# Optimization experiments

Hardware: AMD Instinct MI355X
Metric: run time of the kernel (lower is better)

The kernel has to match this reference:

```python
import jax, jax.numpy as jnp
import numpy as np

BATCH, SEQ, IN, HID = 32, 1024, 512, 1024


def setup_inputs() -> dict:
    key = jax.random.key(0)
    std = 1.0 / np.sqrt(HID)
    ks = jax.random.split(key, 16)
    u = lambda k, shape: jax.random.uniform(k, shape, jnp.float32, -std, std)
    return {
        "x": jax.random.normal(ks[0], (BATCH, SEQ, IN), jnp.float32),
        "Wi": u(ks[1], (IN, 2 * HID)),
        "Wh": u(ks[2], (HID, 2 * HID)),
        "B": u(ks[3], (2 * HID,)),
        "Wni": u(ks[4], (IN, HID)),
        "Wnh": u(ks[5], (HID, HID)),
        "Bni": u(ks[6], (HID,)),
        "Bnh": u(ks[7], (HID,)),
        "Winvi": u(ks[8], (IN, 2 * HID)),
        "Winvh": u(ks[9], (HID, 2 * HID)),
        "Binv": u(ks[10], (2 * HID,)),
        "Wninvi": u(ks[11], (IN, HID)),
        "Wninvh": u(ks[12], (HID, HID)),
        "Bninvi": u(ks[13], (HID,)),
        "Bninvh": u(ks[14], (HID,)),
    }


def _gru_scan(x, Wi, Wh, Bg, Wni, Wnh, Bni, Bnh, reverse):
    # x: [B,S,I]; precompute input projections once (same math, batched GEMM)
    H = Wnh.shape[0]
    gi = jnp.einsum('bsi,ig->bsg', x, Wi) + Bg   # [B,S,2H]
    ni = jnp.einsum('bsi,ih->bsh', x, Wni) + Bni # [B,S,H]
    h0 = jnp.zeros((x.shape[0], H), x.dtype)

    def step(h, inp):
        g_t, n_t = inp                        # [B,2H], [B,H]
        gates = g_t + h @ Wh
        r = jax.nn.sigmoid(gates[:, :H])
        z = jax.nn.sigmoid(gates[:, H:])
        n = jnp.tanh(n_t + r * (h @ Wnh + Bnh))
        h = (1 - z) * n + z * h
        return h, h

    hT, hs = jax.lax.scan(step, h0, (gi.swapaxes(0, 1), ni.swapaxes(0, 1)),
                          reverse=reverse)
    return hs.swapaxes(0, 1), hT              # [B,S,H], [B,H]


def reference(x, Wi, Wh, B, Wni, Wnh, Bni, Bnh,
              Winvi, Winvh, Binv, Wninvi, Wninvh, Bninvi, Bninvh):
    out_f, h_f = _gru_scan(x, Wi, Wh, B, Wni, Wnh, Bni, Bnh, reverse=False)
    out_b, h_b = _gru_scan(x, Winvi, Winvh, Binv, Wninvi, Wninvh, Bninvi, Bninvh,
                           reverse=True)
    output = jnp.concatenate([out_f, out_b], axis=-1)  # [B,S,2H]
    ht = jnp.concatenate([h_f, h_b], axis=-1)          # [B,2H]
    return output, ht
```

## Files before the change

kernel.cpp:

```cpp
#include <hip/hip_runtime.h>
#include <cstdint>
#include <cstddef>

typedef __attribute__((ext_vector_type(8))) short s8v;
typedef __attribute__((ext_vector_type(4))) float f4v;
typedef __attribute__((ext_vector_type(4))) unsigned int u4v;

#define DEVFN __device__ __forceinline__

DEVFN unsigned short f2bf(float f) {
    unsigned int u = __builtin_bit_cast(unsigned int, f);
    return (unsigned short)((u + 0x7FFFu + ((u >> 16) & 1u)) >> 16);
}
DEVFN float bf2f(unsigned short h) {
    unsigned int u = ((unsigned int)h) << 16;
    return __builtin_bit_cast(float, u);
}
DEVFN float sigm(float x) { return 1.0f / (1.0f + __expf(-x)); }
DEVFN float tanh_fast(float x) { float e = __expf(2.0f * x); return 1.0f - 2.0f / (e + 1.0f); }

DEVFN u4v pack8(const unsigned short o[8]) {
    u4v v;
    v[0] = (unsigned)o[0] | ((unsigned)o[1] << 16);
    v[1] = (unsigned)o[2] | ((unsigned)o[3] << 16);
    v[2] = (unsigned)o[4] | ((unsigned)o[5] << 16);
    v[3] = (unsigned)o[6] | ((unsigned)o[7] << 16);
    return v;
}

DEVFN void store_wt(unsigned int* p, unsigned int v) {
    asm volatile("global_store_dword %0, %1, off sc0 sc1"
                 :: "v"(p), "v"(v) : "memory");
}
DEVFN unsigned poll_load(const unsigned int* p) {
    unsigned v;
    asm volatile("global_load_dword %0, %1, off sc0 sc1\n\t"
                 "s_waitcnt vmcnt(0)"
                 : "=v"(v) : "v"(p) : "memory");
    return v;
}
DEVFN void gather_h(const void* p0, const void* p1,
                    u4v& a0, u4v& a1, u4v& a2, u4v& a3,
                    u4v& a4, u4v& a5, u4v& a6, u4v& a7) {
    asm volatile(
        "global_load_dwordx4 %0, %8, off sc0 sc1\n\t"
        "global_load_dwordx4 %1, %8, off offset:1024 sc0 sc1\n\t"
        "global_load_dwordx4 %2, %8, off offset:2048 sc0 sc1\n\t"
        "global_load_dwordx4 %3, %8, off offset:3072 sc0 sc1\n\t"
        "global_load_dwordx4 %4, %9, off sc0 sc1\n\t"
        "global_load_dwordx4 %5, %9, off offset:1024 sc0 sc1\n\t"
        "global_load_dwordx4 %6, %9, off offset:2048 sc0 sc1\n\t"
        "global_load_dwordx4 %7, %9, off offset:3072 sc0 sc1\n\t"
        "s_waitcnt vmcnt(0)"
        : "=&v"(a0), "=&v"(a1), "=&v"(a2), "=&v"(a3),
          "=&v"(a4), "=&v"(a5), "=&v"(a6), "=&v"(a7)
        : "v"(p0), "v"(p1)
        : "memory");
}

constexpr int BB = 32, SS = 1024, II = 512, HH = 1024;
constexpr int NCOL = 6144;

constexpr size_t OFF_X    = 0;
constexpr size_t SZ_X     = (size_t)BB * SS * II * 2;
constexpr size_t OFF_WINT = OFF_X + SZ_X;
constexpr size_t SZ_WINT  = (size_t)NCOL * II * 2;
constexpr size_t OFF_WREC = OFF_WINT + SZ_WINT;
constexpr size_t SZ_WREC  = (size_t)2 * 3072 * HH * 2;
constexpr size_t OFF_BIAS = OFF_WREC + SZ_WREC;
constexpr size_t SZ_BIAS  = (size_t)NCOL * 4;
constexpr size_t OFF_H    = OFF_BIAS + SZ_BIAS;
constexpr size_t SZ_H     = (size_t)2 * 2 * 2 * 64 * 512;
constexpr size_t OFF_BAR  = OFF_H + SZ_H;
constexpr size_t SZ_BAR   = 4096;
constexpr size_t OFF_G    = OFF_BAR + SZ_BAR;
constexpr size_t SZ_G     = (size_t)SS * BB * NCOL * 2;
constexpr size_t WS_NEED  = OFF_G + SZ_G;

constexpr int WL_OFF = 0;
constexpr int PL_OFF = 98304;
constexpr int GR_OFF = 124416;
constexpr int PF_OFF = 130560;
constexpr int RD_OFF = 130592;
constexpr int PG_OFF = 130608;
constexpr int SMEM_TOT = 130624;
constexpr int PLF = 4 * 3 * 16 * 17;

__global__ void prep_kernel(
    const float* __restrict__ x,
    const float* __restrict__ Wi, const float* __restrict__ Wni,
    const float* __restrict__ Winvi, const float* __restrict__ Wninvi,
    const float* __restrict__ Wh, const float* __restrict__ Wnh,
    const float* __restrict__ Winvh, const float* __restrict__ Wninvh,
    const float* __restrict__ Bg, const float* __restrict__ Bni,
    const float* __restrict__ Binv, const float* __restrict__ Bninvi,
    unsigned short* __restrict__ xb, unsigned short* __restrict__ WinT,
    unsigned short* __restrict__ Wrec, float* __restrict__ bias)
{
    constexpr int NX8  = (BB * SS * II) / 8;
    constexpr int NWI8 = (NCOL * II) / 8;
    constexpr int NWR8 = (2 * 3072 * HH) / 8;
    constexpr int TOT  = NX8 + NWI8 + NWR8 + NCOL;
    for (int i = blockIdx.x * blockDim.x + threadIdx.x; i < TOT;
         i += gridDim.x * blockDim.x) {
        if (i < NX8) {
            const float* sp = x + (size_t)i * 8;
            unsigned short o[8];
#pragma unroll
            for (int j = 0; j < 8; ++j) o[j] = f2bf(sp[j]);
            *(u4v*)(xb + (size_t)i * 8) = pack8(o);
        } else if (i < NX8 + NWI8) {
            int u = i - NX8;
            int n = u >> 6, k0 = (u & 63) * 8;
            const float* src; int stride;
            if (n < 2048)      { src = Wi + n;            stride = 2048; }
            else if (n < 3072) { src = Wni + (n - 2048);  stride = 1024; }
            else if (n < 5120) { src = Winvi + (n - 3072); stride = 2048; }
            else               { src = Wninvi + (n - 5120); stride = 1024; }
            unsigned short o[8];
#pragma unroll
            for (int j = 0; j < 8; ++j) o[j] = f2bf(src[(size_t)(k0 + j) * stride]);
            *(u4v*)(WinT + (size_t)n * 512 + k0) = pack8(o);
        } else if (i < NX8 + NWI8 + NWR8) {
            int u = i - NX8 - NWI8;
            int R = u >> 7, k0 = (u & 127) * 8;
            int dir = R / 3072, n = R % 3072;
            const float* src; int stride;
            if (n < 2048) { src = (dir ? Winvh : Wh) + n;          stride = 2048; }
            else          { src = (dir ? Wninvh : Wnh) + (n - 2048); stride = 1024; }
            unsigned short o[8];
#pragma unroll
            for (int j = 0; j < 8; ++j) o[j] = f2bf(src[(size_t)(k0 + j) * stride]);
            *(u4v*)(Wrec + (size_t)R * 1024 + k0) = pack8(o);
        } else {
            int c = i - NX8 - NWI8 - NWR8;
            int dir = c / 3072, cc = c % 3072;
            bias[c] = (cc < 2048) ? (dir ? Binv : Bg)[cc]
                                  : (dir ? Bninvi : Bni)[cc - 2048];
        }
    }
}

#define GLL16(gp, lp) __builtin_amdgcn_global_load_lds( \
    (const __attribute__((address_space(1))) void*)(gp), \
    (__attribute__((address_space(3))) void*)(lp), 16, 0, 0)

__global__ __launch_bounds__(256, 2) void gemm_in(
    const unsigned short* __restrict__ xb,
    const unsigned short* __restrict__ WinT,
    const float* __restrict__ bias,
    unsigned short* __restrict__ G)
{
    __shared__ char smem[32768];
    char* As = smem;
    char* Bs = smem + 16384;
    const int tid = threadIdx.x, lane = tid & 63, wid = tid >> 6;
    int wg = blockIdx.x;
    int swz = (wg & 7) * 1536 + (wg >> 3);
    const int m0 = (swz & 255) * 128, n0 = (swz >> 8) * 128;
    const int l15 = lane & 15, hi = lane >> 4;
    const int mw = (wid & 1) * 64, nw = (wid >> 1) * 64;

    f4v acc[4][4] = {};

    const char* xrow = (const char*)xb;
    const char* wrow = (const char*)WinT;

    for (int kt = 0; kt < 8; ++kt) {
        const int kb0 = kt * 128;
#pragma unroll
        for (int r = 0; r < 4; ++r) {
            int q = wid * 4 + r;
            int o = q * 1024 + lane * 16;
            int row = o >> 7;
            int kbs = (o ^ ((row & 7) << 4)) & 127;
            GLL16(xrow + (size_t)(m0 + row) * 1024 + kb0 + kbs, As + q * 1024);
            GLL16(wrow + (size_t)(n0 + row) * 1024 + kb0 + kbs, Bs + q * 1024);
        }
        __syncthreads();
#pragma unroll
        for (int kc = 0; kc < 2; ++kc) {
            s8v a[4], b[4];
#pragma unroll
            for (int mt = 0; mt < 4; ++mt) {
                int row = mw + mt * 16 + l15;
                int off = (row << 7) + kc * 64 + hi * 16;
                a[mt] = *(const s8v*)(As + (off ^ ((row & 7) << 4)));
            }
#pragma unroll
            for (int nt = 0; nt < 4; ++nt) {
                int row = nw + nt * 16 + l15;
                int off = (row << 7) + kc * 64 + hi * 16;
                b[nt] = *(const s8v*)(Bs + (off ^ ((row & 7) << 4)));
            }
#pragma unroll
            for (int mt = 0; mt < 4; ++mt)
#pragma unroll
                for (int nt = 0; nt < 4; ++nt)
                    acc[mt][nt] = __builtin_amdgcn_mfma_f32_16x16x32_bf16(
                        a[mt], b[nt], acc[mt][nt], 0, 0, 0);
        }
        __syncthreads();
    }
#pragma unroll
    for (int mt = 0; mt < 4; ++mt) {
#pragma unroll
        for (int rg = 0; rg < 4; ++rg) {
            int m = m0 + mw + mt * 16 + hi * 4 + rg;
            int bi = m >> 10, si = m & 1023;
            int bg = bi >> 4, b16 = bi & 15;
#pragma unroll
            for (int nt = 0; nt < 4; ++nt) {
                int n = n0 + nw + nt * 16 + l15;
                int dir = (n >= 3072);
                int rem = n - dir * 3072;
                int gate = rem >> 10, col = rem & 1023;
                int jg = col >> 4, j = col & 15;
                size_t idx = (((((size_t)si * 2 + dir) * 64 + jg) * 2 + bg) * 16
                              + b16) * 48 + gate * 16 + j;
                G[idx] = f2bf(acc[mt][nt][rg] + bias[n]);
            }
        }
    }
}

__global__ __launch_bounds__(320, 1) void gru_rec(
    const unsigned short* __restrict__ G,
    const unsigned short* __restrict__ Wrec,
    const float* __restrict__ Bnh,
    const float* __restrict__ Bninvh,
    unsigned short* __restrict__ hbuf,
    float* __restrict__ out,
    unsigned int* __restrict__ flags)
{
    extern __shared__ char smem[];
    char* wl = smem + WL_OFF;
    float* pl = (float*)(smem + PL_OFF);
    unsigned short* gring = (unsigned short*)(smem + GR_OFF);
    volatile int* pflag = (volatile int*)(smem + PF_OFF);
    volatile int* gready = (volatile int*)(smem + RD_OFF);
    volatile int* gprog  = (volatile int*)(smem + PG_OFF);

    const int tid = threadIdx.x, lane = tid & 63, wid = tid >> 6;
    const int bid = blockIdx.x;
    const int dir = bid >> 7, bg = (bid >> 6) & 1, jg = bid & 63;
    const int jbase = jg * 16, bb = bg * 16;
    const int l15 = lane & 15, hi = lane >> 4;
    unsigned int* fl = flags + ((dir * 2 + bg) << 8);

    if (tid < 4) { gready[tid] = -1; gprog[tid] = -1; }
    if (tid >= 4 && tid < 12) pflag[tid - 4] = -1;
    if (tid < 256) {
        const char* wsrc = (const char*)Wrec;
        for (int q = 0; q < 24; ++q) {
            int o = (q * 256 + tid) * 16;
            int c = o >> 11;
            int kb = (o ^ ((c & 7) << 4)) & 2047;
            int n = dir * 3072 + (c >> 4) * 1024 + jbase + (c & 15);
            *(u4v*)(wl + o) = *(const u4v*)(wsrc + (size_t)n * 2048 + kb);
        }
    }
    const int b_l = tid >> 4, j_l = tid & 15;
    const float bnh = (dir ? Bninvh : Bnh)[jbase + (j_l & 15)];
    __syncthreads();

    const size_t gstride_b = (size_t)2 * 64 * 2 * 768 * 2;
    const char* gcb = (const char*)G + (((size_t)dir * 64 + jg) * 2 + bg) * 1536;

    if (wid == 4) {
        char* grb = (char*)gring;
        for (int t = 0; t < 1024; ++t) {
            const int slot = t & 3;
            if (t >= 4) {
                int v;
                do { v = gprog[lane & 3]; } while (!__all(v >= t - 4));
            }
            const int gpos = dir ? (1023 - t) : t;
            const char* src = gcb + (size_t)gpos * gstride_b + lane * 32;
            if (lane < 48) {
                u4v d0 = *(const u4v*)(src);
                u4v d1 = *(const u4v*)(src + 16);
                *(u4v*)(grb + slot * 1536 + lane * 32) = d0;
                *(u4v*)(grb + slot * 1536 + lane * 32 + 16) = d1;
            }
            asm volatile("s_waitcnt lgkmcnt(0) vmcnt(0)" ::: "memory");
            if (lane == 0) gready[slot] = t;
        }
        return;
    }

    float h_old = 0.0f;
    unsigned int* hbuf32 = (unsigned int*)hbuf;

    for (int s = 0; s < 1024; ++s) {
        const int par = s & 1;
        float* plc = pl + par * PLF;

        const int slot = s & 3;
        {
            int r;
            do { r = gready[slot]; } while (r != s);
        }
        asm volatile("" ::: "memory");
        const int gb = slot * 768 + b_l * 48 + j_l;
        unsigned short gr = gring[gb];
        unsigned short gz = gring[gb + 16];
        unsigned short gn = gring[gb + 32];
        asm volatile("s_waitcnt lgkmcnt(0)" ::: "memory");
        if (lane == 0) gprog[wid] = s;

        float rsum = 0.f, zsum = 0.f, nsum = 0.f;
        if (s > 0) {
            const unsigned tgt = (unsigned)s;
            const unsigned int* fp = fl + wid * 64 + lane;
            unsigned v;
            do { v = poll_load(fp); } while (!__all(v >= tgt));

            const int rbuf = par ^ 1;
            const char* hb = (const char*)hbuf +
                ((((size_t)(dir * 2 + rbuf) * 2 + bg) * 64)
                 + (size_t)(wid * 16 + (hi >> 1))) * 512
                + l15 * 32 + (hi & 1) * 16;
            u4v u[8];
            gather_h(hb, hb + 4096, u[0], u[1], u[2], u[3],
                     u[4], u[5], u[6], u[7]);

            f4v acc[3] = {};
#pragma unroll
            for (int p = 0; p < 3; ++p) {
                int c = p * 16 + l15;
                int cbase = c << 11;
                int sw = (c & 7) << 4;
#pragma unroll
                for (int kc = 0; kc < 8; ++kc) {
                    int off = cbase + (wid << 9) + kc * 64 + hi * 16;
                    s8v bf = *(const s8v*)(wl + (off ^ sw));
                    acc[p] = __builtin_amdgcn_mfma_f32_16x16x32_bf16(
                        __builtin_bit_cast(s8v, u[kc]), bf, acc[p], 0, 0, 0);
                }
            }
#pragma unroll
            for (int p = 0; p < 3; ++p)
#pragma unroll
                for (int rg = 0; rg < 4; ++rg)
                    plc[((wid * 3 + p) * 16 + hi * 4 + rg) * 17 + l15] = acc[p][rg];
            asm volatile("s_waitcnt lgkmcnt(0)" ::: "memory");
            if (lane == 0) pflag[par * 4 + wid] = s;

            {
                int f0, f1, f2, f3;
                do {
                    f0 = pflag[par * 4 + 0]; f1 = pflag[par * 4 + 1];
                    f2 = pflag[par * 4 + 2]; f3 = pflag[par * 4 + 3];
                } while (f0 < s || f1 < s || f2 < s || f3 < s);
            }
            asm volatile("" ::: "memory");
#pragma unroll
            for (int w = 0; w < 4; ++w) {
                rsum += plc[((w * 3 + 0) * 16 + b_l) * 17 + j_l];
                zsum += plc[((w * 3 + 1) * 16 + b_l) * 17 + j_l];
                nsum += plc[((w * 3 + 2) * 16 + b_l) * 17 + j_l];
            }
        }

        float rv = sigm(rsum + bf2f(gr));
        float zv = sigm(zsum + bf2f(gz));
        float nv = tanh_fast(bf2f(gn) + rv * (nsum + bnh));
        float hn = (1.0f - zv) * nv + zv * h_old;
        h_old = hn;

        if (s < 1023) {
            unsigned short hbv = f2bf(hn);
            unsigned int other = (unsigned int)(unsigned short)__shfl_xor((int)hbv, 1);
            if (!(tid & 1)) {
                size_t w32 = ((((size_t)(dir * 2 + par) * 2 + bg) * 64 + jg) * 128)
                             + b_l * 8 + (j_l >> 1);
                store_wt(hbuf32 + w32, (unsigned)hbv | (other << 16));
            }
            asm volatile("s_waitcnt vmcnt(0)" ::: "memory");
            if (lane == 0)
                store_wt(&fl[jg * 4 + wid], (unsigned)(s + 1));
        }

        const int s_out = dir ? (1023 - s) : s;
        __builtin_nontemporal_store(hn,
            &out[((size_t)(bb + b_l) * SS + s_out) * 2048 + dir * 1024 + jbase + j_l]);
        if (s == 1023)
            __builtin_nontemporal_store(hn,
                &out[(size_t)BB * SS * 2048 + (size_t)(bb + b_l) * 2048 +
                     dir * 1024 + jbase + j_l]);
    }
}

extern "C" void kernel_launch(void* const* d_in, const int* in_sizes, int n_in,
                              void* d_out, int out_size, void* d_ws, size_t ws_size,
                              hipStream_t stream)
{
    if (n_in < 15) return;
    const float* x      = (const float*)d_in[0];
    const float* Wi     = (const float*)d_in[1];
    const float* Wh     = (const float*)d_in[2];
    const float* Bg     = (const float*)d_in[3];
    const float* Wni    = (const float*)d_in[4];
    const float* Wnh    = (const float*)d_in[5];
    const float* Bni    = (const float*)d_in[6];
    const float* Bnh    = (const float*)d_in[7];
    const float* Winvi  = (const float*)d_in[8];
    const float* Winvh  = (const float*)d_in[9];
    const float* Binv   = (const float*)d_in[10];
    const float* Wninvi = (const float*)d_in[11];
    const float* Wninvh = (const float*)d_in[12];
    const float* Bninvi = (const float*)d_in[13];
    const float* Bninvh = (const float*)d_in[14];

    if (ws_size < WS_NEED) {
        hipMemsetAsync(d_out, 0, (size_t)out_size * 4, stream);
        return;
    }
    char* ws = (char*)d_ws;
    unsigned short* xb   = (unsigned short*)(ws + OFF_X);
    unsigned short* WinT = (unsigned short*)(ws + OFF_WINT);
    unsigned short* Wrec = (unsigned short*)(ws + OFF_WREC);
    float*          bias = (float*)(ws + OFF_BIAS);
    unsigned short* hbuf = (unsigned short*)(ws + OFF_H);
    unsigned int*   bar  = (unsigned int*)(ws + OFF_BAR);
    unsigned short* G    = (unsigned short*)(ws + OFF_G);

    hipMemsetAsync(ws + OFF_BAR, 0, SZ_BAR, stream);

    prep_kernel<<<4096, 256, 0, stream>>>(
        x, Wi, Wni, Winvi, Wninvi, Wh, Wnh, Winvh, Wninvh,
        Bg, Bni, Binv, Bninvi, xb, WinT, Wrec, bias);

    gemm_in<<<12288, 256, 0, stream>>>(xb, WinT, bias, G);

    hipFuncSetAttribute(reinterpret_cast<const void*>(&gru_rec),
                        hipFuncAttributeMaxDynamicSharedMemorySize, SMEM_TOT);
    gru_rec<<<256, 320, SMEM_TOT, stream>>>(
        G, Wrec, Bnh, Bninvh, hbuf, (float*)d_out, bar);
}
```

Measured before the change: 3.851 ms.

## Double-buffer input GEMM, relayout G, batch output stores, vectorize flag polling

The input-projection GEMM now double-buffers its LDS tiles so the next k-tile's async loads overlap the current MFMA work, and it writes G with nontemporal stores in a simpler [s,dir,gate,b,col] layout. The recurrent kernel's loader wave is changed to gather from that new layout. Flag polling now reads four flags per lane with one dwordx4 load, and hidden outputs are staged in LDS and flushed every 16 steps so the serial loop issues fewer global stores. The prep kernel's weight transpose now converts one element per thread, giving coalesced reads but scalar 2-byte writes. This adds about 16 KB of LDS to the recurrent kernel.

After: 4.181 ms. 8.6% more time.

```diff
diff --git a/kernel.cpp b/kernel.cpp
--- a/kernel.cpp
+++ b/kernel.cpp
@@ -19,22 +19,13 @@
 DEVFN float sigm(float x) { return 1.0f / (1.0f + __expf(-x)); }
 DEVFN float tanh_fast(float x) { float e = __expf(2.0f * x); return 1.0f - 2.0f / (e + 1.0f); }
 
-DEVFN u4v pack8(const unsigned short o[8]) {
-    u4v v;
-    v[0] = (unsigned)o[0] | ((unsigned)o[1] << 16);
-    v[1] = (unsigned)o[2] | ((unsigned)o[3] << 16);
-    v[2] = (unsigned)o[4] | ((unsigned)o[5] << 16);
-    v[3] = (unsigned)o[6] | ((unsigned)o[7] << 16);
-    return v;
-}
-
 DEVFN void store_wt(unsigned int* p, unsigned int v) {
     asm volatile("global_store_dword %0, %1, off sc0 sc1"
                  :: "v"(p), "v"(v) : "memory");
 }
-DEVFN unsigned poll_load(const unsigned int* p) {
-    unsigned v;
-    asm volatile("global_load_dword %0, %1, off sc0 sc1\n\t"
+DEVFN u4v poll_load4(const unsigned int* p) {
+    u4v v;
+    asm volatile("global_load_dwordx4 %0, %1, off sc0 sc1\n\t"
                  "s_waitcnt vmcnt(0)"
                  : "=v"(v) : "v"(p) : "memory");
     return v;
@@ -83,7 +74,8 @@
 constexpr int PF_OFF = 130560;
 constexpr int RD_OFF = 130592;
 constexpr int PG_OFF = 130608;
-constexpr int SMEM_TOT = 130624;
+constexpr int OB_OFF = 130624;
+constexpr int SMEM_TOT = 147008;
 constexpr int PLF = 4 * 3 * 16 * 17;
 
 __global__ void prep_kernel(
@@ -97,10 +89,11 @@
     unsigned short* __restrict__ xb, unsigned short* __restrict__ WinT,
     unsigned short* __restrict__ Wrec, float* __restrict__ bias)
 {
-    constexpr int NX8  = (BB * SS * II) / 8;
-    constexpr int NWI8 = (NCOL * II) / 8;
-    constexpr int NWR8 = (2 * 3072 * HH) / 8;
-    constexpr int TOT  = NX8 + NWI8 + NWR8 + NCOL;
+    typedef __attribute__((ext_vector_type(4))) unsigned int uv4;
+    constexpr int NX8 = (BB * SS * II) / 8;
+    constexpr int NWI = NCOL * II;
+    constexpr int NWR = NCOL * HH;
+    constexpr int TOT = NX8 + NWI + NWR + NCOL;
     for (int i = blockIdx.x * blockDim.x + threadIdx.x; i < TOT;
          i += gridDim.x * blockDim.x) {
         if (i < NX8) {
@@ -108,32 +101,31 @@
             unsigned short o[8];
 #pragma unroll
             for (int j = 0; j < 8; ++j) o[j] = f2bf(sp[j]);
-            *(u4v*)(xb + (size_t)i * 8) = pack8(o);
-        } else if (i < NX8 + NWI8) {
+            uv4 v;
+            v[0] = (unsigned)o[0] | ((unsigned)o[1] << 16);
+            v[1] = (unsigned)o[2] | ((unsigned)o[3] << 16);
+            v[2] = (unsigned)o[4] | ((unsigned)o[5] << 16);
+            v[3] = (unsigned)o[6] | ((unsigned)o[7] << 16);
+            *(uv4*)(xb + (size_t)i * 8) = v;
+        } else if (i < NX8 + NWI) {
             int u = i - NX8;
-            int n = u >> 6, k0 = (u & 63) * 8;
-            const float* src; int stride;
-            if (n < 2048)      { src = Wi + n;            stride = 2048; }
-            else if (n < 3072) { src = Wni + (n - 2048);  stride = 1024; }
-            else if (n < 5120) { src = Winvi + (n - 3072); stride = 2048; }
-            else               { src = Wninvi + (n - 5120); stride = 1024; }
-            unsigned short o[8];
-#pragma unroll
-            for (int j = 0; j < 8; ++j) o[j] = f2bf(src[(size_t)(k0 + j) * stride]);
-            *(u4v*)(WinT + (size_t)n * 512 + k0) = pack8(o);
-        } else if (i < NX8 + NWI8 + NWR8) {
-            int u = i - NX8 - NWI8;
-            int R = u >> 7, k0 = (u & 127) * 8;
-            int dir = R / 3072, n = R % 3072;
-            const float* src; int stride;
-            if (n < 2048) { src = (dir ? Winvh : Wh) + n;          stride = 2048; }
-            else          { src = (dir ? Wninvh : Wnh) + (n - 2048); stride = 1024; }
-            unsigned short o[8];
-#pragma unroll
-            for (int j = 0; j < 8; ++j) o[j] = f2bf(src[(size_t)(k0 + j) * stride]);
-            *(u4v*)(Wrec + (size_t)R * 1024 + k0) = pack8(o);
+            int k = u / NCOL, n = u % NCOL;
+            const float* src; int stride, col;
+            if (n < 2048)      { src = Wi;     col = n;        stride = 2048; }
+            else if (n < 3072) { src = Wni;    col = n - 2048; stride = 1024; }
+            else if (n < 5120) { src = Winvi;  col = n - 3072; stride = 2048; }
+            else               { src = Wninvi; col = n - 5120; stride = 1024; }
+            WinT[(size_t)n * 512 + k] = f2bf(src[(size_t)k * stride + col]);
+        } else if (i < NX8 + NWI + NWR) {
+            int u = i - NX8 - NWI;
+            int k = u / NCOL, R = u % NCOL;
+            int dir = R / 3072, rr = R % 3072;
+            const float* src; int stride, col;
+            if (rr < 2048) { src = dir ? Winvh : Wh;   col = rr;        stride = 2048; }
+            else           { src = dir ? Wninvh : Wnh; col = rr - 2048; stride = 1024; }
+            Wrec[(size_t)R * 1024 + k] = f2bf(src[(size_t)k * stride + col]);
         } else {
-            int c = i - NX8 - NWI8 - NWR8;
+            int c = i - NX8 - NWI - NWR;
             int dir = c / 3072, cc = c % 3072;
             bias[c] = (cc < 2048) ? (dir ? Binv : Bg)[cc]
                                   : (dir ? Bninvi : Bni)[cc - 2048];
@@ -151,9 +143,7 @@
     const float* __restrict__ bias,
     unsigned short* __restrict__ G)
 {
-    __shared__ char smem[32768];
-    char* As = smem;
-    char* Bs = smem + 16384;
+    __shared__ char smem[65536];
     const int tid = threadIdx.x, lane = tid & 63, wid = tid >> 6;
     int wg = blockIdx.x;
     int swz = (wg & 7) * 1536 + (wg >> 3);
@@ -162,11 +152,12 @@
     const int mw = (wid & 1) * 64, nw = (wid >> 1) * 64;
 
     f4v acc[4][4] = {};
-
     const char* xrow = (const char*)xb;
     const char* wrow = (const char*)WinT;
 
-    for (int kt = 0; kt < 8; ++kt) {
+    auto stage = [&](int buf, int kt) {
+        char* As = smem + buf * 32768;
+        char* Bs = As + 16384;
         const int kb0 = kt * 128;
 #pragma unroll
         for (int r = 0; r < 4; ++r) {
@@ -177,7 +168,15 @@
             GLL16(xrow + (size_t)(m0 + row) * 1024 + kb0 + kbs, As + q * 1024);
             GLL16(wrow + (size_t)(n0 + row) * 1024 + kb0 + kbs, Bs + q * 1024);
         }
-        __syncthreads();
+    };
+
+    stage(0, 0);
+    __syncthreads();
+    int buf = 0;
+    for (int kt = 0; kt < 8; ++kt) {
+        if (kt < 7) stage(buf ^ 1, kt + 1);
+        char* As = smem + buf * 32768;
+        char* Bs = As + 16384;
 #pragma unroll
         for (int kc = 0; kc < 2; ++kc) {
             s8v a[4], b[4];
@@ -201,6 +200,7 @@
                         a[mt], b[nt], acc[mt][nt], 0, 0, 0);
         }
         __syncthreads();
+        buf ^= 1;
     }
 #pragma unroll
     for (int mt = 0; mt < 4; ++mt) {
@@ -208,17 +208,14 @@
         for (int rg = 0; rg < 4; ++rg) {
             int m = m0 + mw + mt * 16 + hi * 4 + rg;
             int bi = m >> 10, si = m & 1023;
-            int bg = bi >> 4, b16 = bi & 15;
 #pragma unroll
             for (int nt = 0; nt < 4; ++nt) {
                 int n = n0 + nw + nt * 16 + l15;
                 int dir = (n >= 3072);
                 int rem = n - dir * 3072;
                 int gate = rem >> 10, col = rem & 1023;
-                int jg = col >> 4, j = col & 15;
-                size_t idx = (((((size_t)si * 2 + dir) * 64 + jg) * 2 + bg) * 16
-                              + b16) * 48 + gate * 16 + j;
-                G[idx] = f2bf(acc[mt][nt][rg] + bias[n]);
+                size_t idx = ((((size_t)si * 2 + dir) * 3 + gate) * 32 + bi) * 1024 + col;
+                __builtin_nontemporal_store(f2bf(acc[mt][nt][rg] + bias[n]), &G[idx]);
             }
         }
     }
@@ -240,6 +237,7 @@
     volatile int* pflag = (volatile int*)(smem + PF_OFF);
     volatile int* gready = (volatile int*)(smem + RD_OFF);
     volatile int* gprog  = (volatile int*)(smem + PG_OFF);
+    float* obuf = (float*)(smem + OB_OFF);
 
     const int tid = threadIdx.x, lane = tid & 63, wid = tid >> 6;
     const int bid = blockIdx.x;
@@ -264,11 +262,12 @@
     const float bnh = (dir ? Bninvh : Bnh)[jbase + (j_l & 15)];
     __syncthreads();
 
-    const size_t gstride_b = (size_t)2 * 64 * 2 * 768 * 2;
-    const char* gcb = (const char*)G + (((size_t)dir * 64 + jg) * 2 + bg) * 1536;
-
     if (wid == 4) {
         char* grb = (char*)gring;
+        const char* gdir = (const char*)G + (size_t)dir * 196608;
+        const int g8 = lane >> 4, bsel = lane & 15;
+        const size_t lsoff = (((size_t)g8 * 32 + bb + bsel) * 1024 + jbase) * 2;
+        const int ldoff = (bsel * 48 + g8 * 16) * 2;
         for (int t = 0; t < 1024; ++t) {
             const int slot = t & 3;
             if (t >= 4) {
@@ -276,12 +275,12 @@
                 do { v = gprog[lane & 3]; } while (!__all(v >= t - 4));
             }
             const int gpos = dir ? (1023 - t) : t;
-            const char* src = gcb + (size_t)gpos * gstride_b + lane * 32;
             if (lane < 48) {
+                const char* src = gdir + (size_t)gpos * 393216 + lsoff;
                 u4v d0 = *(const u4v*)(src);
                 u4v d1 = *(const u4v*)(src + 16);
-                *(u4v*)(grb + slot * 1536 + lane * 32) = d0;
-                *(u4v*)(grb + slot * 1536 + lane * 32 + 16) = d1;
+                *(u4v*)(grb + slot * 1536 + ldoff) = d0;
+                *(u4v*)(grb + slot * 1536 + ldoff + 16) = d1;
             }
             asm volatile("s_waitcnt lgkmcnt(0) vmcnt(0)" ::: "memory");
             if (lane == 0) gready[slot] = t;
@@ -312,9 +311,12 @@
         float rsum = 0.f, zsum = 0.f, nsum = 0.f;
         if (s > 0) {
             const unsigned tgt = (unsigned)s;
-            const unsigned int* fp = fl + wid * 64 + lane;
-            unsigned v;
-            do { v = poll_load(fp); } while (!__all(v >= tgt));
+            const unsigned int* fp = fl + (lane << 2);
+            u4v fv;
+            do {
+                fv = poll_load4(fp);
+            } while (!__all(fv[0] >= tgt && fv[1] >= tgt &&
+                            fv[2] >= tgt && fv[3] >= tgt));
 
             const int rbuf = par ^ 1;
             const char* hb = (const char*)hbuf +
@@ -382,9 +384,19 @@
                 store_wt(&fl[jg * 4 + wid], (unsigned)(s + 1));
         }
 
-        const int s_out = dir ? (1023 - s) : s;
-        __builtin_nontemporal_store(hn,
-            &out[((size_t)(bb + b_l) * SS + s_out) * 2048 + dir * 1024 + jbase + j_l]);
+        obuf[(s & 15) * 256 + tid] = hn;
+        if ((s & 15) == 15) {
+            const int s0 = s - 15;
+#pragma unroll
+            for (int k = 0; k < 16; ++k) {
+                float v = obuf[k * 256 + tid];
+                int st = s0 + k;
+                int s_out = dir ? (1023 - st) : st;
+                __builtin_nontemporal_store(v,
+                    &out[((size_t)(bb + b_l) * SS + s_out) * 2048
+                         + dir * 1024 + jbase + j_l]);
+            }
+        }
         if (s == 1023)
             __builtin_nontemporal_store(hn,
                 &out[(size_t)BB * SS * 2048 + (size_t)(bb + b_l) * 2048 +
```
